# Kernel tuning notes

Hardware: AMD Instinct MI355X
Metric: run time of the kernel (lower is better)

The kernel has to match this reference:

```python
import jax, jax.numpy as jnp
import numpy as np

NB_LABELS = 10
NB_EDGE_LABELS = 3
SINKHORN_ITERS = 10


def setup_inputs() -> dict:
    key = jax.random.key(0)
    k1, k2, k3, k4, k5, k6 = jax.random.split(key, 6)
    n = m = 95
    nb_node_pairs = NB_LABELS * (NB_LABELS - 1) // 2
    nb_edge_pairs = NB_EDGE_LABELS * (NB_EDGE_LABELS - 1) // 2
    node_weights = 0.1 * 1.1 * jax.random.uniform(k1, (nb_node_pairs + 1,), jnp.float32)
    node_weights = node_weights.at[-1].set(0.3)
    edge_weights = 0.1 * 1.1 * jax.random.uniform(k2, (nb_edge_pairs + 1,), jnp.float32)
    edge_weights = edge_weights.at[-1].set(0.2)
    A_g1 = jax.random.randint(k3, (n * n,), 0, NB_EDGE_LABELS + 1, jnp.int32)
    A_g2 = jax.random.randint(k4, (m * m,), 0, NB_EDGE_LABELS + 1, jnp.int32)
    labels1 = jax.random.randint(k5, (n,), 0, NB_LABELS, jnp.int32)
    labels2 = jax.random.randint(k6, (m,), 0, NB_LABELS, jnp.int32)
    return dict(node_weights=node_weights, edge_weights=edge_weights,
                A_g1=A_g1, A_g2=A_g2, labels1=labels1, labels2=labels2, n=n, m=m)


def _from_weights_to_costs(node_weights, edge_weights):
    cn = jax.nn.relu(node_weights)
    ce = jax.nn.relu(edge_weights)
    node_ins_del, edge_ins_del = cn[-1], ce[-1]
    iu = jnp.triu_indices(NB_LABELS, k=1)
    node_costs = jnp.zeros((NB_LABELS, NB_LABELS), jnp.float32).at[iu].set(cn[:-1])
    node_costs = node_costs + node_costs.T
    iue = jnp.triu_indices(NB_EDGE_LABELS, k=1)
    edge_costs = jnp.zeros((NB_EDGE_LABELS, NB_EDGE_LABELS), jnp.float32).at[iue].set(ce[:-1])
    edge_costs = edge_costs + edge_costs.T  # zero diagonal => k != l handled for free
    return node_costs, node_ins_del, edge_costs, edge_ins_del


def _kron_perm(X4, n1, m1):
    # torch cat/unbind trick: out[j*m1+k, i*m1+l] = X4[i, j, k, l]
    return X4.transpose(1, 2, 0, 3).reshape(n1 * m1, n1 * m1)


def _sinkhorn(S, iters):
    # eps_assign2: alternate row/col normalization, last row/col scale fixed to 1
    def step(S, _):
        rs = (1.0 / S.sum(axis=1)).at[-1].set(1.0)
        S = S * rs[:, None]
        cs = (1.0 / S.sum(axis=0)).at[-1].set(1.0)
        S = S * cs[None, :]
        return S, None
    S, _ = jax.lax.scan(step, S, None, length=iters)
    return S


def _ged_forward(node_weights, edge_weights, A_g1, A_g2, labels1, labels2, n, m):
    node_costs, node_ins_del, edge_costs, edge_ins_del = _from_weights_to_costs(node_weights, edge_weights)
    n1, m1 = n + 1, m + 1
    N = n1 * m1
    A1 = jnp.zeros((n1, n1), jnp.int32).at[:n, :n].set(A_g1[:n * n].reshape(n, n))
    A2 = jnp.zeros((m1, m1), jnp.int32).at[:m, :m].set(A_g2[:m * m].reshape(m, m))
    Ab1, Ab2 = A1 != 0, A2 != 0
    # edge insertion/deletion costs: XOR of edge presence, Kronecker-expanded
    ins_del = jnp.logical_xor(Ab1[:, :, None, None], Ab2[None, None, :, :]).astype(jnp.float32)
    C = edge_ins_del * _kron_perm(ins_del, n1, m1)
    # edge substitution: one-hot over edge labels, contracted with symmetric edge_costs (zero diag)
    labs = jnp.arange(1, NB_EDGE_LABELS + 1, dtype=jnp.int32)
    E1 = (A1[None, :, :] == labs[:, None, None]).astype(jnp.float32)  # [L, n1, n1]
    E2 = (A2[None, :, :] == labs[:, None, None]).astype(jnp.float32)  # [L, m1, m1]
    Csub = jnp.einsum('aij,bkl,ab->ijkl', E1, E2, edge_costs)
    C = C + _kron_perm(Csub, n1, m1)
    # node cost vector D (diagonal of C)
    Dnm = node_costs[labels1[:n][:, None], labels2[:m][None, :]]  # [n, m]
    D2 = jnp.full((n1, m1), node_ins_del, jnp.float32)
    D2 = D2.at[:n, :m].set(Dnm)
    D2 = D2.at[n, m].set(0.0)
    c = D2.reshape(-1)  # length N
    diag_idx = jnp.arange(N)
    C = C.at[diag_idx, diag_idx].set(c)
    Dmat = C.at[diag_idx, diag_idx].set(0.0)  # C - eye * diag(C)
    # Sinkhorn-like soft assignment
    S = _sinkhorn(jnp.exp(-0.5 * c.reshape(n1, m1)), SINKHORN_ITERS)
    v = S.reshape(-1)
    ged = 0.5 * (v @ (Dmat @ v)) + c @ v
    return ged


def reference(node_weights, edge_weights, A_g1, A_g2, labels1, labels2, n, m):
    return _ged_forward(node_weights, edge_weights, A_g1, A_g2, labels1, labels2, n, m)
```

## Files before the change

### kernel.cpp

```cpp
#include <hip/hip_runtime.h>

#define NV 95
#define SINK_ITERS 10

__global__ __launch_bounds__(1024)
void ged_all(const float* __restrict__ nw, const float* __restrict__ ew,
             const int* __restrict__ Ag1, const int* __restrict__ Ag2,
             const int* __restrict__ lab1g, const int* __restrict__ lab2g,
             float* __restrict__ outp)
{
    __shared__ float cn[46], ce[4];
    __shared__ float nc[100];
    __shared__ float ftab[16];
    __shared__ float nids;
    __shared__ int   labs1[96], labs2[96];
    __shared__ int   cnt1[12], cnt2[12];
    __shared__ int   P1h[3 * 121], P2h[3 * 121];
    __shared__ int   H1[4 * 12], H2[4 * 12];
    __shared__ float E0s[11 * 12];
    __shared__ float Rs[12], Cs[12];
    __shared__ float Ts[11 * 12];
    __shared__ float P1f[4 * 121], P2f[4 * 121];
    __shared__ float Q1s[4 * 132], R2s[4 * 132];
    __shared__ float wred[16];

    const int tid = threadIdx.x;

    if (tid < 46) cn[tid] = fmaxf(nw[tid], 0.f);
    if (tid >= 64 && tid < 68) ce[tid - 64] = fmaxf(ew[tid - 64], 0.f);
    if (tid >= 128 && tid < 224) { int t = tid - 128; labs1[t] = (t < NV) ? lab1g[t] : 10; }
    if (tid >= 256 && tid < 352) { int t = tid - 256; labs2[t] = (t < NV) ? lab2g[t] : 10; }
    for (int i = tid; i < 363; i += 1024) { P1h[i] = 0; P2h[i] = 0; }
    if (tid < 48) { H1[tid] = 0; H2[tid] = 0; }
    if (tid < 12) { cnt1[tid] = 0; cnt2[tid] = 0; }
    __syncthreads();

    if (tid < 45) {
        int i = 0, rem = tid;
        while (rem >= 9 - i) { rem -= 9 - i; ++i; }
        int j = i + 1 + rem;
        float v = cn[tid];
        nc[i * 10 + j] = v; nc[j * 10 + i] = v;
    }
    if (tid >= 45 && tid < 55) nc[(tid - 45) * 11] = 0.f;
    if (tid == 0) {
        nids = cn[45];
        float e01 = ce[0], e02 = ce[1], e12 = ce[2], eid = ce[3];
        ftab[0] = 0.f;  ftab[1] = eid;  ftab[2] = eid;  ftab[3] = eid;
        ftab[4] = eid;  ftab[5] = 0.f;  ftab[6] = e01;  ftab[7] = e02;
        ftab[8] = eid;  ftab[9] = e01;  ftab[10] = 0.f; ftab[11] = e12;
        ftab[12] = eid; ftab[13] = e02; ftab[14] = e12; ftab[15] = 0.f;
    }
    if (tid == 1) { cnt1[10] = 1; cnt2[10] = 1; }
    if (tid >= 64 && tid < 64 + NV)   atomicAdd(&cnt1[labs1[tid - 64]], 1);
    if (tid >= 192 && tid < 192 + NV) atomicAdd(&cnt2[labs2[tid - 192]], 1);
    if (tid >= 320 && tid < 416) {
        int u = tid - 320;
        int e = (u < NV) ? Ag1[u * 96] : 0;
        atomicAdd(&H1[e * 12 + labs1[u]], 1);
    }
    if (tid >= 448 && tid < 544) {
        int u = tid - 448;
        int e = (u < NV) ? Ag2[u * 96] : 0;
        atomicAdd(&H2[e * 12 + labs2[u]], 1);
    }
    for (int idx = tid; idx < NV * NV; idx += 1024) {
        int i = idx / NV, j = idx - i * NV;
        int v1 = Ag1[idx];
        if (v1) atomicAdd(&P1h[(v1 - 1) * 121 + labs1[i] * 11 + labs1[j]], 1);
        int v2 = Ag2[idx];
        if (v2) atomicAdd(&P2h[(v2 - 1) * 121 + labs2[i] * 11 + labs2[j]], 1);
    }
    __syncthreads();

    if (tid < 121) {
        int a = tid / 11, b = tid - a * 11;
        float c;
        if (a < 10 && b < 10) c = nc[a * 10 + b];
        else c = (a == 10 && b == 10) ? 0.f : nids;
        E0s[a * 12 + b] = expf(-0.5f * c);
    }
    if (tid < 484) {
        int e = tid / 121, aa = tid - e * 121;
        float v;
        if (e == 0) v = (float)(cnt1[aa / 11] * cnt1[aa % 11])
                        - (float)(P1h[aa] + P1h[121 + aa] + P1h[242 + aa]);
        else v = (float)P1h[(e - 1) * 121 + aa];
        P1f[tid] = v;
    }
    if (tid >= 512 && tid < 996) {
        int t = tid - 512;
        int e = t / 121, aa = t - e * 121;
        float v;
        if (e == 0) v = (float)(cnt2[aa / 11] * cnt2[aa % 11])
                        - (float)(P2h[aa] + P2h[121 + aa] + P2h[242 + aa]);
        else v = (float)P2h[(e - 1) * 121 + aa];
        P2f[t] = v;
    }
    __syncthreads();

    if (tid < 64) {
        int l = tid;
        int ll = (l < 11) ? l : 0;
        float ecrow[11], eccol[11];
        #pragma unroll
        for (int b = 0; b < 11; ++b) ecrow[b] = E0s[ll * 12 + b] * (float)cnt2[b];
        #pragma unroll
        for (int a = 0; a < 11; ++a) eccol[a] = E0s[a * 12 + ll] * (float)cnt1[a];
        float Rv = 1.f, Cv = 1.f;
        for (int it = 0; it < SINK_ITERS; ++it) {
            float s = 0.f;
            #pragma unroll
            for (int b = 0; b < 11; ++b) s += ecrow[b] * __shfl(Cv, b, 64);
            Rv = (l == 10) ? 1.f : 1.f / s;
            float s2 = 0.f;
            #pragma unroll
            for (int a = 0; a < 11; ++a) s2 += eccol[a] * __shfl(Rv, a, 64);
            Cv = (l == 10) ? 1.f : 1.f / s2;
        }
        if (l < 11) { Rs[l] = Rv; Cs[l] = Cv; }
    }
    __syncthreads();

    if (tid < 121) {
        int a = tid / 11, b = tid - a * 11;
        Ts[a * 12 + b] = E0s[a * 12 + b] * Rs[a] * Cs[b];
    }
    __syncthreads();

    if (tid < 484) {
        int e = tid / 121, ab = tid - e * 121, a = ab / 11, b = ab - a * 11;
        float s = 0.f;
        #pragma unroll
        for (int a2 = 0; a2 < 11; ++a2) s += P1f[e * 121 + a * 11 + a2] * Ts[a2 * 12 + b];
        Q1s[e * 132 + a * 12 + b] = s;
    }
    if (tid >= 512 && tid < 996) {
        int t = tid - 512;
        int e = t / 121, ab = t - e * 121, a = ab / 11, b = ab - a * 11;
        float s = 0.f;
        #pragma unroll
        for (int b2 = 0; b2 < 11; ++b2) s += P2f[e * 121 + b * 11 + b2] * Ts[a * 12 + b2];
        R2s[e * 132 + a * 12 + b] = s;
    }
    __syncthreads();

    float x = 0.f;
    if (tid < 968) {
        #pragma unroll
        for (int r = 0; r < 2; ++r) {
            int t = tid + r * 968;
            int p = t / 121, ab = t - p * 121;
            int e1 = p >> 2, e2 = p & 3;
            int a = ab / 11, b = ab - a * 11;
            float f  = ftab[p];
            float tt = Ts[a * 12 + b];
            x += 0.5f * f * (Q1s[e1 * 132 + a * 12 + b] * R2s[e2 * 132 + a * 12 + b]
                             - (float)H1[e1 * 12 + a] * (float)H2[e2 * 12 + b] * tt * tt);
        }
    }
    if (tid < 121) {
        int a = tid / 11, b = tid - a * 11;
        float c;
        if (a < 10 && b < 10) c = nc[a * 10 + b];
        else c = (a == 10 && b == 10) ? 0.f : nids;
        x += (float)(cnt1[a] * cnt2[b]) * c * Ts[a * 12 + b];
    }
    #pragma unroll
    for (int off = 32; off > 0; off >>= 1) x += __shfl_down(x, off, 64);
    if ((tid & 63) == 0) wred[tid >> 6] = x;
    __syncthreads();
    if (tid == 0) {
        float s = 0.f;
        #pragma unroll
        for (int w = 0; w < 16; ++w) s += wred[w];
        outp[0] = s;
    }
}

extern "C" void kernel_launch(void* const* d_in, const int* in_sizes, int n_in,
                              void* d_out, int out_size, void* d_ws, size_t ws_size,
                              hipStream_t stream)
{
    (void)in_sizes; (void)n_in; (void)out_size; (void)d_ws; (void)ws_size;
    const float* nw  = (const float*)d_in[0];
    const float* ew  = (const float*)d_in[1];
    const int*   Ag1 = (const int*)d_in[2];
    const int*   Ag2 = (const int*)d_in[3];
    const int*   l1  = (const int*)d_in[4];
    const int*   l2  = (const int*)d_in[5];
    hipLaunchKernelGGL(ged_all, dim3(1), dim3(1024), 0, stream,
                       nw, ew, Ag1, Ag2, l1, l2, (float*)d_out);
}
```

Measured before the change: 14.76 us.

## Overlap Sinkhorn with adjacency histogram scan and hoist vectorized adjacency loads

The adjacency matrices are now prefetched as int4 vectors into registers at kernel start, and the pair-label histogram atomics are moved into the same phase as the Sinkhorn iteration. Wave 0 runs Sinkhorn (computing exp costs inline), other threads build E0s and scan the adjacency, so two barrier phases are removed. The P-float and T intermediate arrays are eliminated by computing them on the fly in later phases. In exchange, register pressure rises and the later loops do some redundant recomputation.

After: 14.40 us. -2.4%, faster.

```diff
diff --git a/kernel.cpp b/kernel.cpp
--- a/kernel.cpp
+++ b/kernel.cpp
@@ -19,12 +19,28 @@
     __shared__ int   H1[4 * 12], H2[4 * 12];
     __shared__ float E0s[11 * 12];
     __shared__ float Rs[12], Cs[12];
-    __shared__ float Ts[11 * 12];
-    __shared__ float P1f[4 * 121], P2f[4 * 121];
     __shared__ float Q1s[4 * 132], R2s[4 * 132];
     __shared__ float wred[16];
 
     const int tid = threadIdx.x;
+
+    const int4* A1_4 = (const int4*)Ag1;
+    const int4* A2_4 = (const int4*)Ag2;
+    int4 a1r[3], a2r[3];
+    const bool scanner = (tid >= 192);
+    const int  sbase = tid - 192;
+    if (scanner) {
+        #pragma unroll
+        for (int r = 0; r < 3; ++r) {
+            int slot = sbase + r * 832;
+            if (slot < 2256) { a1r[r] = A1_4[slot]; a2r[r] = A2_4[slot]; }
+        }
+    }
+    int rem1 = 0, rem2 = 0;
+    if (tid == 1023) { rem1 = Ag1[9024]; rem2 = Ag2[9024]; }
+    int d1 = 0, d2 = 0;
+    if (tid >= 320 && tid < 416) { int u = tid - 320; d1 = (u < NV) ? Ag1[u * 96] : 0; }
+    if (tid >= 448 && tid < 544) { int u = tid - 448; d2 = (u < NV) ? Ag2[u * 96] : 0; }
 
     if (tid < 46) cn[tid] = fmaxf(nw[tid], 0.f);
     if (tid >= 64 && tid < 68) ce[tid - 64] = fmaxf(ew[tid - 64], 0.f);
@@ -54,59 +70,27 @@
     if (tid == 1) { cnt1[10] = 1; cnt2[10] = 1; }
     if (tid >= 64 && tid < 64 + NV)   atomicAdd(&cnt1[labs1[tid - 64]], 1);
     if (tid >= 192 && tid < 192 + NV) atomicAdd(&cnt2[labs2[tid - 192]], 1);
-    if (tid >= 320 && tid < 416) {
-        int u = tid - 320;
-        int e = (u < NV) ? Ag1[u * 96] : 0;
-        atomicAdd(&H1[e * 12 + labs1[u]], 1);
-    }
-    if (tid >= 448 && tid < 544) {
-        int u = tid - 448;
-        int e = (u < NV) ? Ag2[u * 96] : 0;
-        atomicAdd(&H2[e * 12 + labs2[u]], 1);
-    }
-    for (int idx = tid; idx < NV * NV; idx += 1024) {
-        int i = idx / NV, j = idx - i * NV;
-        int v1 = Ag1[idx];
-        if (v1) atomicAdd(&P1h[(v1 - 1) * 121 + labs1[i] * 11 + labs1[j]], 1);
-        int v2 = Ag2[idx];
-        if (v2) atomicAdd(&P2h[(v2 - 1) * 121 + labs2[i] * 11 + labs2[j]], 1);
-    }
-    __syncthreads();
-
-    if (tid < 121) {
-        int a = tid / 11, b = tid - a * 11;
-        float c;
-        if (a < 10 && b < 10) c = nc[a * 10 + b];
-        else c = (a == 10 && b == 10) ? 0.f : nids;
-        E0s[a * 12 + b] = expf(-0.5f * c);
-    }
-    if (tid < 484) {
-        int e = tid / 121, aa = tid - e * 121;
-        float v;
-        if (e == 0) v = (float)(cnt1[aa / 11] * cnt1[aa % 11])
-                        - (float)(P1h[aa] + P1h[121 + aa] + P1h[242 + aa]);
-        else v = (float)P1h[(e - 1) * 121 + aa];
-        P1f[tid] = v;
-    }
-    if (tid >= 512 && tid < 996) {
-        int t = tid - 512;
-        int e = t / 121, aa = t - e * 121;
-        float v;
-        if (e == 0) v = (float)(cnt2[aa / 11] * cnt2[aa % 11])
-                        - (float)(P2h[aa] + P2h[121 + aa] + P2h[242 + aa]);
-        else v = (float)P2h[(e - 1) * 121 + aa];
-        P2f[t] = v;
-    }
+    if (tid >= 320 && tid < 416) atomicAdd(&H1[d1 * 12 + labs1[tid - 320]], 1);
+    if (tid >= 448 && tid < 544) atomicAdd(&H2[d2 * 12 + labs2[tid - 448]], 1);
     __syncthreads();
 
     if (tid < 64) {
         int l = tid;
         int ll = (l < 11) ? l : 0;
+        float nid_l = nids;
         float ecrow[11], eccol[11];
         #pragma unroll
-        for (int b = 0; b < 11; ++b) ecrow[b] = E0s[ll * 12 + b] * (float)cnt2[b];
-        #pragma unroll
-        for (int a = 0; a < 11; ++a) eccol[a] = E0s[a * 12 + ll] * (float)cnt1[a];
+        for (int b = 0; b < 11; ++b) {
+            float c = (ll < 10 && b < 10) ? nc[ll * 10 + b]
+                     : ((ll == 10 && b == 10) ? 0.f : nid_l);
+            ecrow[b] = expf(-0.5f * c) * (float)cnt2[b];
+        }
+        #pragma unroll
+        for (int a = 0; a < 11; ++a) {
+            float c = (a < 10 && ll < 10) ? nc[a * 10 + ll]
+                     : ((a == 10 && ll == 10) ? 0.f : nid_l);
+            eccol[a] = expf(-0.5f * c) * (float)cnt1[a];
+        }
         float Rv = 1.f, Cv = 1.f;
         for (int it = 0; it < SINK_ITERS; ++it) {
             float s = 0.f;
@@ -119,12 +103,33 @@
             Cv = (l == 10) ? 1.f : 1.f / s2;
         }
         if (l < 11) { Rs[l] = Rv; Cs[l] = Cv; }
-    }
-    __syncthreads();
-
-    if (tid < 121) {
-        int a = tid / 11, b = tid - a * 11;
-        Ts[a * 12 + b] = E0s[a * 12 + b] * Rs[a] * Cs[b];
+    } else if (tid < 185) {
+        int t = tid - 64;
+        int a = t / 11, b = t - a * 11;
+        float c = (a < 10 && b < 10) ? nc[a * 10 + b]
+                 : ((a == 10 && b == 10) ? 0.f : nids);
+        E0s[a * 12 + b] = expf(-0.5f * c);
+    } else if (scanner) {
+        #pragma unroll
+        for (int r = 0; r < 3; ++r) {
+            int slot = sbase + r * 832;
+            if (slot < 2256) {
+                int base = slot * 4;
+                int v1[4] = { a1r[r].x, a1r[r].y, a1r[r].z, a1r[r].w };
+                int v2[4] = { a2r[r].x, a2r[r].y, a2r[r].z, a2r[r].w };
+                #pragma unroll
+                for (int q = 0; q < 4; ++q) {
+                    int idx = base + q;
+                    int i = idx / NV, j = idx - i * NV;
+                    if (v1[q]) atomicAdd(&P1h[(v1[q] - 1) * 121 + labs1[i] * 11 + labs1[j]], 1);
+                    if (v2[q]) atomicAdd(&P2h[(v2[q] - 1) * 121 + labs2[i] * 11 + labs2[j]], 1);
+                }
+            }
+        }
+        if (tid == 1023) {
+            if (rem1) atomicAdd(&P1h[(rem1 - 1) * 121 + labs1[94] * 11 + labs1[94]], 1);
+            if (rem2) atomicAdd(&P2h[(rem2 - 1) * 121 + labs2[94] * 11 + labs2[94]], 1);
+        }
     }
     __syncthreads();
 
@@ -132,16 +137,28 @@
         int e = tid / 121, ab = tid - e * 121, a = ab / 11, b = ab - a * 11;
         float s = 0.f;
         #pragma unroll
-        for (int a2 = 0; a2 < 11; ++a2) s += P1f[e * 121 + a * 11 + a2] * Ts[a2 * 12 + b];
-        Q1s[e * 132 + a * 12 + b] = s;
+        for (int a2 = 0; a2 < 11; ++a2) {
+            int aa = a * 11 + a2;
+            float p = (e == 0)
+                ? (float)(cnt1[a] * cnt1[a2] - P1h[aa] - P1h[121 + aa] - P1h[242 + aa])
+                : (float)P1h[(e - 1) * 121 + aa];
+            s += p * E0s[a2 * 12 + b] * Rs[a2];
+        }
+        Q1s[e * 132 + a * 12 + b] = s * Cs[b];
     }
     if (tid >= 512 && tid < 996) {
         int t = tid - 512;
         int e = t / 121, ab = t - e * 121, a = ab / 11, b = ab - a * 11;
         float s = 0.f;
         #pragma unroll
-        for (int b2 = 0; b2 < 11; ++b2) s += P2f[e * 121 + b * 11 + b2] * Ts[a * 12 + b2];
-        R2s[e * 132 + a * 12 + b] = s;
+        for (int b2 = 0; b2 < 11; ++b2) {
+            int bb = b * 11 + b2;
+            float p = (e == 0)
+                ? (float)(cnt2[b] * cnt2[b2] - P2h[bb] - P2h[121 + bb] - P2h[242 + bb])
+                : (float)P2h[(e - 1) * 121 + bb];
+            s += p * E0s[a * 12 + b2] * Cs[b2];
+        }
+        R2s[e * 132 + a * 12 + b] = s * Rs[a];
     }
     __syncthreads();
 
@@ -154,17 +171,16 @@
             int e1 = p >> 2, e2 = p & 3;
             int a = ab / 11, b = ab - a * 11;
             float f  = ftab[p];
-            float tt = Ts[a * 12 + b];
+            float tt = E0s[a * 12 + b] * Rs[a] * Cs[b];
             x += 0.5f * f * (Q1s[e1 * 132 + a * 12 + b] * R2s[e2 * 132 + a * 12 + b]
                              - (float)H1[e1 * 12 + a] * (float)H2[e2 * 12 + b] * tt * tt);
         }
     }
     if (tid < 121) {
         int a = tid / 11, b = tid - a * 11;
-        float c;
-        if (a < 10 && b < 10) c = nc[a * 10 + b];
-        else c = (a == 10 && b == 10) ? 0.f : nids;
-        x += (float)(cnt1[a] * cnt2[b]) * c * Ts[a * 12 + b];
+        float c = (a < 10 && b < 10) ? nc[a * 10 + b]
+                 : ((a == 10 && b == 10) ? 0.f : nids);
+        x += (float)(cnt1[a] * cnt2[b]) * c * E0s[a * 12 + b] * Rs[a] * Cs[b];
     }
     #pragma unroll
     for (int off = 32; off > 0; off >>= 1) x += __shfl_down(x, off, 64);
```
